# Kernel optimization log

Measured on AMD Instinct MI355X. Metric: run time of the kernel, lower is better.

Reference implementation:

```python
import jax, jax.numpy as jnp
import numpy as np

N_NODES = 100000
N_EDGES = 800000
NODE_DIM = 128
HIDDEN = 256
OUT_DIM = 512
N_LAYERS = 4
N_GRAPHS = 64


def _linear_init(key, out_f, in_f):
    kw, kb = jax.random.split(key)
    bound = 1.0 / np.sqrt(in_f)
    w = jax.random.uniform(kw, (out_f, in_f), jnp.float32, -bound, bound)
    b = jax.random.uniform(kb, (out_f,), jnp.float32, -bound, bound)
    return w, b


def setup_inputs() -> dict:
    key = jax.random.key(0)
    ks = jax.random.split(key, 16)
    x = jax.random.normal(ks[0], (N_NODES, NODE_DIM), jnp.float32)
    edge_index = jax.random.randint(ks[1], (2, N_EDGES), 0, N_NODES, jnp.int64)
    batch = jnp.sort(jax.random.randint(ks[2], (N_NODES,), 0, N_GRAPHS, jnp.int64))
    node_w, node_b = _linear_init(ks[3], HIDDEN, NODE_DIM)
    gw1, gb1, gw2, gb2 = [], [], [], []
    for i in range(N_LAYERS):
        w1, b1 = _linear_init(ks[4 + 2 * i], HIDDEN, HIDDEN)
        w2, b2 = _linear_init(ks[5 + 2 * i], HIDDEN, HIDDEN)
        gw1.append(w1); gb1.append(b1); gw2.append(w2); gb2.append(b2)
    gin_w1 = jnp.stack(gw1); gin_b1 = jnp.stack(gb1)
    gin_w2 = jnp.stack(gw2); gin_b2 = jnp.stack(gb2)
    eps = jnp.zeros((N_LAYERS,), jnp.float32)  # train_eps init 0
    out_w1, out_b1 = _linear_init(ks[12], HIDDEN, HIDDEN)
    out_w2, out_b2 = _linear_init(ks[13], OUT_DIM, HIDDEN)
    return {
        "x": x, "edge_index": edge_index, "batch": batch,
        "node_w": node_w, "node_b": node_b,
        "gin_w1": gin_w1, "gin_b1": gin_b1,
        "gin_w2": gin_w2, "gin_b2": gin_b2, "eps": eps,
        "out_w1": out_w1, "out_b1": out_b1,
        "out_w2": out_w2, "out_b2": out_b2,
    }


def reference(x, edge_index, batch, node_w, node_b, gin_w1, gin_b1, gin_w2,
              gin_b2, eps, out_w1, out_b1, out_w2, out_b2):
    src, dst = edge_index[0], edge_index[1]
    # node projection + relu
    h = jax.nn.relu(x @ node_w.T + node_b)  # [N, H]
    for i in range(N_LAYERS):
        # GINConv: mlp((1+eps)*x + sum_{j in N(i)} x_j); x_j = h[src], agg at dst
        agg = jax.ops.segment_sum(h[src], dst, num_segments=N_NODES)
        z = (1.0 + eps[i]) * h + agg
        z = jax.nn.relu(z @ gin_w1[i].T + gin_b1[i])
        z = z @ gin_w2[i].T + gin_b2[i]
        h = jax.nn.relu(z)  # outer relu in forward
    # global_mean_pool over batch assignment
    counts = jax.ops.segment_sum(jnp.ones((N_NODES,), h.dtype), batch,
                                 num_segments=N_GRAPHS)
    sums = jax.ops.segment_sum(h, batch, num_segments=N_GRAPHS)
    h_graph = sums / jnp.maximum(counts, 1.0)[:, None]  # [B, H]
    out = jax.nn.relu(h_graph @ out_w1.T + out_b1) @ out_w2.T + out_b2
    return out  # [B, OUT_DIM]
```

## Files before the change

kernel.cpp:

```cpp
#include <hip/hip_runtime.h>
#include <stdint.h>

#define N_NODES   100000
#define N_EDGES   800000
#define NODE_DIM  128
#define HIDDEN    256
#define OUT_DIM   512
#define N_LAYERS  4
#define N_GRAPHS  64
#define POOL_CHUNKS 8
#define SCAN_BLK  1024
#define SCAN_NB   ((N_NODES + SCAN_BLK - 1) / SCAN_BLK)

typedef _Float16 f16;
typedef __attribute__((ext_vector_type(8))) _Float16 f16x8;
typedef __attribute__((ext_vector_type(4))) _Float16 f16x4;
typedef __attribute__((ext_vector_type(4))) float    f32x4;

__global__ void k_f2h(const float* __restrict__ in, f16* __restrict__ out, int n4) {
    int i = blockIdx.x * 256 + threadIdx.x;
    if (i < n4) {
        f32x4 v = *(const f32x4*)(in + (size_t)i * 4);
        f16x4 o;
        o[0] = (f16)v[0]; o[1] = (f16)v[1]; o[2] = (f16)v[2]; o[3] = (f16)v[3];
        *(f16x4*)(out + (size_t)i * 4) = o;
    }
}

__global__ void k_hist(const int* __restrict__ ei, int* __restrict__ deg) {
    int e = blockIdx.x * 256 + threadIdx.x;
    if (e < N_EDGES) atomicAdd(&deg[ei[N_EDGES + e]], 1);
}

__global__ __launch_bounds__(1024) void k_scan1(const int* __restrict__ deg,
                                                int* __restrict__ rowptr,
                                                int* __restrict__ bsums) {
    __shared__ int tmp[SCAN_BLK];
    int tid = threadIdx.x;
    int i = blockIdx.x * SCAN_BLK + tid;
    int v = (i < N_NODES) ? deg[i] : 0;
    tmp[tid] = v;
    __syncthreads();
    for (int off = 1; off < SCAN_BLK; off <<= 1) {
        int t = (tid >= off) ? tmp[tid - off] : 0;
        __syncthreads();
        tmp[tid] += t;
        __syncthreads();
    }
    if (i < N_NODES) rowptr[i] = tmp[tid] - v;
    if (tid == SCAN_BLK - 1) bsums[blockIdx.x] = tmp[tid];
}

__global__ __launch_bounds__(128) void k_scan2(const int* __restrict__ bsums,
                                               int* __restrict__ boffs,
                                               int* __restrict__ rowptr) {
    __shared__ int tmp[128];
    int tid = threadIdx.x;
    int v = (tid < SCAN_NB) ? bsums[tid] : 0;
    tmp[tid] = v;
    __syncthreads();
    for (int off = 1; off < 128; off <<= 1) {
        int t = (tid >= off) ? tmp[tid - off] : 0;
        __syncthreads();
        tmp[tid] += t;
        __syncthreads();
    }
    if (tid < SCAN_NB) boffs[tid] = tmp[tid] - v;
    if (tid == 127) rowptr[N_NODES] = tmp[127];
}

__global__ __launch_bounds__(1024) void k_scan3(int* __restrict__ rowptr,
                                                const int* __restrict__ boffs,
                                                int* __restrict__ cursor) {
    int i = blockIdx.x * SCAN_BLK + threadIdx.x;
    if (i < N_NODES) {
        int r = rowptr[i] + boffs[blockIdx.x];
        rowptr[i] = r;
        cursor[i] = r;
    }
}

__global__ void k_scatter(const int* __restrict__ ei, int* __restrict__ cursor,
                          int* __restrict__ col) {
    int e = blockIdx.x * 256 + threadIdx.x;
    if (e < N_EDGES) {
        int d = ei[N_EDGES + e];
        int p = atomicAdd(&cursor[d], 1);
        col[p] = ei[e];
    }
}

__global__ __launch_bounds__(256) void k_agg(const f16* __restrict__ h,
                                             const int* __restrict__ rowptr,
                                             const int* __restrict__ col,
                                             const float* __restrict__ eps, int layer,
                                             f16* __restrict__ z) {
    int node = blockIdx.x * 4 + (threadIdx.x >> 6);
    if (node >= N_NODES) return;
    int lane = threadIdx.x & 63;
    int half = lane >> 5;
    int c0 = (lane & 31) * 8;
    float e1 = 1.0f + eps[layer];
    float a0 = 0, a1 = 0, a2 = 0, a3 = 0, a4 = 0, a5 = 0, a6 = 0, a7 = 0;
    int jb = rowptr[node], je = rowptr[node + 1];
    int j = jb;
    for (; j + 8 <= je; j += 8) {
        int s0 = col[j     + half];
        int s1 = col[j + 2 + half];
        int s2 = col[j + 4 + half];
        int s3 = col[j + 6 + half];
        f16x8 v0 = *(const f16x8*)(h + (size_t)s0 * HIDDEN + c0);
        f16x8 v1 = *(const f16x8*)(h + (size_t)s1 * HIDDEN + c0);
        f16x8 v2 = *(const f16x8*)(h + (size_t)s2 * HIDDEN + c0);
        f16x8 v3 = *(const f16x8*)(h + (size_t)s3 * HIDDEN + c0);
        a0 += (float)v0[0] + (float)v1[0] + (float)v2[0] + (float)v3[0];
        a1 += (float)v0[1] + (float)v1[1] + (float)v2[1] + (float)v3[1];
        a2 += (float)v0[2] + (float)v1[2] + (float)v2[2] + (float)v3[2];
        a3 += (float)v0[3] + (float)v1[3] + (float)v2[3] + (float)v3[3];
        a4 += (float)v0[4] + (float)v1[4] + (float)v2[4] + (float)v3[4];
        a5 += (float)v0[5] + (float)v1[5] + (float)v2[5] + (float)v3[5];
        a6 += (float)v0[6] + (float)v1[6] + (float)v2[6] + (float)v3[6];
        a7 += (float)v0[7] + (float)v1[7] + (float)v2[7] + (float)v3[7];
    }
    for (; j + 2 <= je; j += 2) {
        int s = col[j + half];
        f16x8 v = *(const f16x8*)(h + (size_t)s * HIDDEN + c0);
        a0 += (float)v[0]; a1 += (float)v[1]; a2 += (float)v[2]; a3 += (float)v[3];
        a4 += (float)v[4]; a5 += (float)v[5]; a6 += (float)v[6]; a7 += (float)v[7];
    }
    if (j < je && half == 0) {
        int s = col[j];
        f16x8 v = *(const f16x8*)(h + (size_t)s * HIDDEN + c0);
        a0 += (float)v[0]; a1 += (float)v[1]; a2 += (float)v[2]; a3 += (float)v[3];
        a4 += (float)v[4]; a5 += (float)v[5]; a6 += (float)v[6]; a7 += (float)v[7];
    }
    if (half == 0) {
        f16x8 hv = *(const f16x8*)(h + (size_t)node * HIDDEN + c0);
        a0 += e1 * (float)hv[0]; a1 += e1 * (float)hv[1];
        a2 += e1 * (float)hv[2]; a3 += e1 * (float)hv[3];
        a4 += e1 * (float)hv[4]; a5 += e1 * (float)hv[5];
        a6 += e1 * (float)hv[6]; a7 += e1 * (float)hv[7];
    }
    a0 += __shfl_xor(a0, 32); a1 += __shfl_xor(a1, 32);
    a2 += __shfl_xor(a2, 32); a3 += __shfl_xor(a3, 32);
    a4 += __shfl_xor(a4, 32); a5 += __shfl_xor(a5, 32);
    a6 += __shfl_xor(a6, 32); a7 += __shfl_xor(a7, 32);
    if (half == 0) {
        f16x8 o;
        o[0] = (f16)a0; o[1] = (f16)a1; o[2] = (f16)a2; o[3] = (f16)a3;
        o[4] = (f16)a4; o[5] = (f16)a5; o[6] = (f16)a6; o[7] = (f16)a7;
        *(f16x8*)(z + (size_t)node * HIDDEN + c0) = o;
    }
}

template<int K>
__global__ __launch_bounds__(512) void k_gemm(const f16* __restrict__ A,
                                              const f16* __restrict__ B,
                                              const float* __restrict__ bias,
                                              f16* __restrict__ C, int nsl16) {
    constexpr int NPANEL = K >> 6;
    constexpr int NKS    = K >> 5;
    __shared__ f16 Bs[NPANEL * 256 * 64];
    const int tid = threadIdx.x, wid = tid >> 6, lane = tid & 63;
    const int klo = lane >> 4;
    const int l15 = lane & 15;

#pragma unroll
    for (int p = 0; p < NPANEL; ++p) {
#pragma unroll
        for (int r = 0; r < 4; ++r) {
            int chunk = (r << 9) + tid;
            int brow = chunk >> 3, c8 = chunk & 7;
            int sc8  = c8 ^ (brow & 7);
            const f16* src = B + (size_t)brow * K + (p << 6) + sc8 * 8;
            f16* dst = Bs + (p << 14) + (size_t)((r << 9) + (wid << 6)) * 8;
            __builtin_amdgcn_global_load_lds((const __attribute__((address_space(1))) void*)src,
                                             (__attribute__((address_space(3))) void*)dst, 16, 0, 0);
        }
    }
    __syncthreads();

    auto loada = [&](f16x8 (&a)[NKS], int slab) {
        const f16* arow = A + (size_t)((slab << 4) + l15) * K + (klo << 3);
#pragma unroll
        for (int ks = 0; ks < NKS; ++ks)
            a[ks] = *(const f16x8*)(arow + (ks << 5));
    };
    auto compute = [&](const f16x8 (&a)[NKS], int slab) {
        f32x4 acc[16] = {};
#pragma unroll
        for (int ks = 0; ks < NKS; ++ks) {
            const int kk = ((ks & 1) << 2) | klo;
            const f16* pb = Bs + ((ks >> 1) << 14);
#pragma unroll
            for (int n = 0; n < 16; ++n) {
                int rb = (n << 4) + l15;
                f16x8 bf = *(const f16x8*)(pb + rb * 64 + ((kk ^ (rb & 7)) << 3));
                acc[n] = __builtin_amdgcn_mfma_f32_16x16x32_f16(a[ks], bf, acc[n], 0, 0, 0);
            }
        }
#pragma unroll
        for (int n = 0; n < 16; ++n) {
            int gc = (n << 4) + l15;
            float bv = bias[gc];
#pragma unroll
            for (int j = 0; j < 4; ++j) {
                int gr = (slab << 4) + (klo << 2) + j;
                float v = fmaxf(acc[n][j] + bv, 0.0f);
                C[(size_t)gr * HIDDEN + gc] = (f16)v;
            }
        }
    };

    const int STRIDE = gridDim.x * 8;
    int s = blockIdx.x * 8 + wid;
    if (s >= nsl16) return;
    f16x8 aA[NKS], aB[NKS];
    loada(aA, s);
    for (;;) {
        int s2 = s + STRIDE;
        if (s2 < nsl16) loada(aB, s2);
        compute(aA, s);
        if (s2 >= nsl16) break;
        int s3 = s2 + STRIDE;
        if (s3 < nsl16) loada(aA, s3);
        compute(aB, s2);
        if (s3 >= nsl16) break;
        s = s3;
    }
}

__global__ void k_bounds(const int* __restrict__ batch, int* __restrict__ starts) {
    int i = blockIdx.x * 256 + threadIdx.x;
    if (i >= N_NODES) return;
    int g  = batch[i];
    int gp = (i == 0) ? -1 : batch[i - 1];
    for (int q = gp + 1; q <= g; ++q) starts[q] = i;
    if (i == N_NODES - 1) {
        for (int q = g + 1; q <= N_GRAPHS; ++q) starts[q] = N_NODES;
    }
}

__global__ __launch_bounds__(256) void k_pool(const f16* __restrict__ h,
                                              const int* __restrict__ starts,
                                              float* __restrict__ part) {
    int g = blockIdx.x, ch = blockIdx.y, c = threadIdx.x;
    int s = starts[g], e = starts[g + 1];
    int len = e - s;
    int per = (len + POOL_CHUNKS - 1) / POOL_CHUNKS;
    int lo = s + ch * per;
    int hi = lo + per; if (hi > e) hi = e;
    float acc = 0.0f;
    for (int n = lo; n < hi; ++n) acc += (float)h[(size_t)n * HIDDEN + c];
    part[((size_t)g * POOL_CHUNKS + ch) * HIDDEN + c] = acc;
}

__global__ __launch_bounds__(256) void k_head(const float* __restrict__ part,
                                              const int* __restrict__ starts,
                                              const float* __restrict__ w1,
                                              const float* __restrict__ b1,
                                              const float* __restrict__ w2,
                                              const float* __restrict__ b2,
                                              float* __restrict__ out) {
    __shared__ float hg[HIDDEN];
    __shared__ float t[HIDDEN];
    int g = blockIdx.x, tid = threadIdx.x;
    int cnti = starts[g + 1] - starts[g];
    float cnt = (float)(cnti > 1 ? cnti : 1);
    float s = 0.0f;
#pragma unroll
    for (int ch = 0; ch < POOL_CHUNKS; ++ch)
        s += part[((size_t)g * POOL_CHUNKS + ch) * HIDDEN + tid];
    hg[tid] = s / cnt;
    __syncthreads();
    float a = b1[tid];
    for (int k = 0; k < HIDDEN; ++k) a += hg[k] * w1[(size_t)tid * HIDDEN + k];
    t[tid] = fmaxf(a, 0.0f);
    __syncthreads();
    for (int j = tid; j < OUT_DIM; j += 256) {
        float o = b2[j];
        for (int k = 0; k < HIDDEN; ++k) o += t[k] * w2[(size_t)j * HIDDEN + k];
        out[(size_t)g * OUT_DIM + j] = o;
    }
}

extern "C" void kernel_launch(void* const* d_in, const int* in_sizes, int n_in,
                              void* d_out, int out_size, void* d_ws, size_t ws_size,
                              hipStream_t stream) {
    const float* x      = (const float*)d_in[0];
    const int*   ei     = (const int*)d_in[1];
    const int*   batch  = (const int*)d_in[2];
    const float* node_w = (const float*)d_in[3];
    const float* node_b = (const float*)d_in[4];
    const float* gw1    = (const float*)d_in[5];
    const float* gb1    = (const float*)d_in[6];
    const float* gw2    = (const float*)d_in[7];
    const float* gb2    = (const float*)d_in[8];
    const float* eps    = (const float*)d_in[9];
    const float* ow1    = (const float*)d_in[10];
    const float* ob1    = (const float*)d_in[11];
    const float* ow2    = (const float*)d_in[12];
    const float* ob2    = (const float*)d_in[13];
    float* out = (float*)d_out;

    char* p = (char*)d_ws;
    auto alloc = [&](size_t bytes) {
        char* r = p;
        p += (bytes + 255) & ~(size_t)255;
        return (void*)r;
    };
    f16* hb   = (f16*)alloc((size_t)N_NODES * HIDDEN * 2);
    f16* zb   = (f16*)alloc((size_t)N_NODES * HIDDEN * 2);
    f16* tb   = (f16*)alloc((size_t)N_NODES * HIDDEN * 2);
    f16* xb   = (f16*)alloc((size_t)N_NODES * NODE_DIM * 2);
    f16* nwb  = (f16*)alloc((size_t)HIDDEN * NODE_DIM * 2);
    f16* w1b  = (f16*)alloc((size_t)N_LAYERS * HIDDEN * HIDDEN * 2);
    f16* w2b  = (f16*)alloc((size_t)N_LAYERS * HIDDEN * HIDDEN * 2);
    int* deg    = (int*)alloc((size_t)N_NODES * 4);
    int* rowptr = (int*)alloc((size_t)(N_NODES + 1) * 4);
    int* cursor = (int*)alloc((size_t)N_NODES * 4);
    int* col    = (int*)alloc((size_t)N_EDGES * 4);
    float* part = (float*)alloc((size_t)N_GRAPHS * POOL_CHUNKS * HIDDEN * 4);
    int* starts = (int*)alloc((size_t)(N_GRAPHS + 1) * 4);
    int* bsums  = (int*)alloc((size_t)SCAN_NB * 4);
    int* boffs  = (int*)alloc((size_t)SCAN_NB * 4);
    (void)in_sizes; (void)n_in; (void)out_size; (void)ws_size;

    hipMemsetAsync(deg, 0, (size_t)N_NODES * 4, stream);

    k_f2h<<<(N_NODES * NODE_DIM / 4 + 255) / 256, 256, 0, stream>>>(x, xb, N_NODES * NODE_DIM / 4);
    k_f2h<<<(HIDDEN * NODE_DIM / 4 + 255) / 256, 256, 0, stream>>>(node_w, nwb, HIDDEN * NODE_DIM / 4);
    k_f2h<<<(N_LAYERS * HIDDEN * HIDDEN / 4 + 255) / 256, 256, 0, stream>>>(gw1, w1b, N_LAYERS * HIDDEN * HIDDEN / 4);
    k_f2h<<<(N_LAYERS * HIDDEN * HIDDEN / 4 + 255) / 256, 256, 0, stream>>>(gw2, w2b, N_LAYERS * HIDDEN * HIDDEN / 4);

    k_hist<<<(N_EDGES + 255) / 256, 256, 0, stream>>>(ei, deg);
    k_scan1<<<SCAN_NB, SCAN_BLK, 0, stream>>>(deg, rowptr, bsums);
    k_scan2<<<1, 128, 0, stream>>>(bsums, boffs, rowptr);
    k_scan3<<<SCAN_NB, SCAN_BLK, 0, stream>>>(rowptr, boffs, cursor);
    k_scatter<<<(N_EDGES + 255) / 256, 256, 0, stream>>>(ei, cursor, col);

    k_bounds<<<(N_NODES + 255) / 256, 256, 0, stream>>>(batch, starts);

    const int NSL16 = N_NODES / 16;
    k_gemm<NODE_DIM><<<256, 512, 0, stream>>>(xb, nwb, node_b, hb, NSL16);

    for (int l = 0; l < N_LAYERS; ++l) {
        k_agg<<<(N_NODES + 3) / 4, 256, 0, stream>>>(hb, rowptr, col, eps, l, zb);
        k_gemm<HIDDEN><<<256, 512, 0, stream>>>(zb, w1b + (size_t)l * HIDDEN * HIDDEN,
                                                gb1 + (size_t)l * HIDDEN, tb, NSL16);
        k_gemm<HIDDEN><<<256, 512, 0, stream>>>(tb, w2b + (size_t)l * HIDDEN * HIDDEN,
                                                gb2 + (size_t)l * HIDDEN, hb, NSL16);
    }

    dim3 pgrid(N_GRAPHS, POOL_CHUNKS);
    k_pool<<<pgrid, 256, 0, stream>>>(hb, starts, part);
    k_head<<<N_GRAPHS, 256, 0, stream>>>(part, starts, ow1, ob1, ow2, ob2, out);
}
```

Baseline: 697.3 us.

## Switch node GEMM to 32x32x16 MFMA tiles with 32-row slabs

The per-wave GEMM now processes 32-row slabs using 32x32x16 MFMA instructions and two column halves, instead of 16-row slabs with 16x16x32 MFMAs. The larger MFMA tile halves the LDS B-fragment reads per flop and improves operand reuse. The software double-buffered A prefetch is removed, so A loads are no longer overlapped with compute. There are also fewer slabs per wave to spread across the grid. N_NODES divides by 32, so no tail handling is needed.

```diff
diff --git a/kernel.cpp b/kernel.cpp
--- a/kernel.cpp
+++ b/kernel.cpp
@@ -13,9 +13,10 @@
 #define SCAN_NB   ((N_NODES + SCAN_BLK - 1) / SCAN_BLK)
 
 typedef _Float16 f16;
-typedef __attribute__((ext_vector_type(8))) _Float16 f16x8;
-typedef __attribute__((ext_vector_type(4))) _Float16 f16x4;
-typedef __attribute__((ext_vector_type(4))) float    f32x4;
+typedef __attribute__((ext_vector_type(8)))  _Float16 f16x8;
+typedef __attribute__((ext_vector_type(4)))  _Float16 f16x4;
+typedef __attribute__((ext_vector_type(4)))  float    f32x4;
+typedef __attribute__((ext_vector_type(16))) float    f32x16;
 
 __global__ void k_f2h(const float* __restrict__ in, f16* __restrict__ out, int n4) {
     int i = blockIdx.x * 256 + threadIdx.x;
@@ -157,13 +158,13 @@
 __global__ __launch_bounds__(512) void k_gemm(const f16* __restrict__ A,
                                               const f16* __restrict__ B,
                                               const float* __restrict__ bias,
-                                              f16* __restrict__ C, int nsl16) {
+                                              f16* __restrict__ C, int nsl32) {
     constexpr int NPANEL = K >> 6;
-    constexpr int NKS    = K >> 5;
+    constexpr int NKS    = K >> 4;
     __shared__ f16 Bs[NPANEL * 256 * 64];
     const int tid = threadIdx.x, wid = tid >> 6, lane = tid & 63;
-    const int klo = lane >> 4;
-    const int l15 = lane & 15;
+    const int hi  = lane >> 5;
+    const int l31 = lane & 31;
 
 #pragma unroll
     for (int p = 0; p < NPANEL; ++p) {
@@ -180,53 +181,39 @@
     }
     __syncthreads();
 
-    auto loada = [&](f16x8 (&a)[NKS], int slab) {
-        const f16* arow = A + (size_t)((slab << 4) + l15) * K + (klo << 3);
+    for (int s = blockIdx.x * 8 + wid; s < nsl32; s += (gridDim.x << 3)) {
+        const int r0 = s << 5;
+        f16x8 a[NKS];
+        const f16* arow = A + (size_t)(r0 + l31) * K + (hi << 3);
 #pragma unroll
         for (int ks = 0; ks < NKS; ++ks)
-            a[ks] = *(const f16x8*)(arow + (ks << 5));
-    };
-    auto compute = [&](const f16x8 (&a)[NKS], int slab) {
-        f32x4 acc[16] = {};
-#pragma unroll
-        for (int ks = 0; ks < NKS; ++ks) {
-            const int kk = ((ks & 1) << 2) | klo;
-            const f16* pb = Bs + ((ks >> 1) << 14);
-#pragma unroll
-            for (int n = 0; n < 16; ++n) {
-                int rb = (n << 4) + l15;
-                f16x8 bf = *(const f16x8*)(pb + rb * 64 + ((kk ^ (rb & 7)) << 3));
-                acc[n] = __builtin_amdgcn_mfma_f32_16x16x32_f16(a[ks], bf, acc[n], 0, 0, 0);
+            a[ks] = *(const f16x8*)(arow + (ks << 4));
+#pragma unroll
+        for (int hf = 0; hf < 2; ++hf) {
+            f32x16 acc[4] = {};
+#pragma unroll
+            for (int ks = 0; ks < NKS; ++ks) {
+                const int kk = ((ks & 3) << 1) | hi;
+                const f16* pb = Bs + ((ks >> 2) << 14);
+#pragma unroll
+                for (int n = 0; n < 4; ++n) {
+                    int rb = (hf << 7) + (n << 5) + l31;
+                    f16x8 bf = *(const f16x8*)(pb + rb * 64 + ((kk ^ (rb & 7)) << 3));
+                    acc[n] = __builtin_amdgcn_mfma_f32_32x32x16_f16(a[ks], bf, acc[n], 0, 0, 0);
+                }
+            }
+#pragma unroll
+            for (int n = 0; n < 4; ++n) {
+                int gc = (hf << 7) + (n << 5) + l31;
+                float bv = bias[gc];
+#pragma unroll
+                for (int reg = 0; reg < 16; ++reg) {
+                    int gr = r0 + (reg & 3) + ((reg >> 2) << 3) + (hi << 2);
+                    float v = fmaxf(acc[n][reg] + bv, 0.0f);
+                    C[(size_t)gr * HIDDEN + gc] = (f16)v;
+                }
             }
         }
-#pragma unroll
-        for (int n = 0; n < 16; ++n) {
-            int gc = (n << 4) + l15;
-            float bv = bias[gc];
-#pragma unroll
-            for (int j = 0; j < 4; ++j) {
-                int gr = (slab << 4) + (klo << 2) + j;
-                float v = fmaxf(acc[n][j] + bv, 0.0f);
-                C[(size_t)gr * HIDDEN + gc] = (f16)v;
-            }
-        }
-    };
-
-    const int STRIDE = gridDim.x * 8;
-    int s = blockIdx.x * 8 + wid;
-    if (s >= nsl16) return;
-    f16x8 aA[NKS], aB[NKS];
-    loada(aA, s);
-    for (;;) {
-        int s2 = s + STRIDE;
-        if (s2 < nsl16) loada(aB, s2);
-        compute(aA, s);
-        if (s2 >= nsl16) break;
-        int s3 = s2 + STRIDE;
-        if (s3 < nsl16) loada(aA, s3);
-        compute(aB, s2);
-        if (s3 >= nsl16) break;
-        s = s3;
     }
 }
 
@@ -341,15 +328,15 @@
 
     k_bounds<<<(N_NODES + 255) / 256, 256, 0, stream>>>(batch, starts);
 
-    const int NSL16 = N_NODES / 16;
-    k_gemm<NODE_DIM><<<256, 512, 0, stream>>>(xb, nwb, node_b, hb, NSL16);
+    const int NSL32 = N_NODES / 32;
+    k_gemm<NODE_DIM><<<256, 512, 0, stream>>>(xb, nwb, node_b, hb, NSL32);
 
     for (int l = 0; l < N_LAYERS; ++l) {
         k_agg<<<(N_NODES + 3) / 4, 256, 0, stream>>>(hb, rowptr, col, eps, l, zb);
         k_gemm<HIDDEN><<<256, 512, 0, stream>>>(zb, w1b + (size_t)l * HIDDEN * HIDDEN,
-                                                gb1 + (size_t)l * HIDDEN, tb, NSL16);
+                                                gb1 + (size_t)l * HIDDEN, tb, NSL32);
         k_gemm<HIDDEN><<<256, 512, 0, stream>>>(tb, w2b + (size_t)l * HIDDEN * HIDDEN,
-                                                gb2 + (size_t)l * HIDDEN, hb, NSL16);
+                                                gb2 + (size_t)l * HIDDEN, hb, NSL32);
     }
 
     dim3 pgrid(N_GRAPHS, POOL_CHUNKS);
```

After: 697.9 us. No clear change (+0.1%).
